# Kernel tuning notes

Hardware: AMD Instinct MI355X
Metric: run time of the kernel (lower is better)

Reference implementation:

```python
import jax, jax.numpy as jnp
import numpy as np

N_ATOMS = 100000
N_BONDS = 200000
N_MOLS = 4000
ATOMS_PER_MOL = 25
MAX_NB = 6
ATOM_FDIM = 133
BOND_FDIM = 14
HIDDEN = 300
DEPTH = 3


def setup_inputs() -> dict:
    key = jax.random.key(0)
    ks = jax.random.split(key, 8)
    f_atoms = jax.random.normal(ks[0], (N_ATOMS, ATOM_FDIM), dtype=jnp.float32)
    f_bonds = jax.random.normal(ks[1], (N_BONDS, BOND_FDIM), dtype=jnp.float32)
    # incoming-bond lists per atom (irregular gather targets)
    a2b = jax.random.randint(ks[2], (N_ATOMS, MAX_NB), 0, N_BONDS, dtype=jnp.int32)
    # source atom of each directed bond
    b2a = jax.random.randint(ks[3], (N_BONDS,), 0, N_ATOMS, dtype=jnp.int32)
    # reverse bond: directed bonds come in pairs (2i, 2i+1)
    b2revb = (jnp.arange(N_BONDS, dtype=jnp.int32) ^ 1)
    # contiguous [start, size] per molecule
    starts = jnp.arange(N_MOLS, dtype=jnp.int32) * ATOMS_PER_MOL
    sizes = jnp.full((N_MOLS,), ATOMS_PER_MOL, dtype=jnp.int32)
    a_scope = jnp.stack([starts, sizes], axis=1)
    W_i = jax.random.normal(ks[4], (HIDDEN, ATOM_FDIM + BOND_FDIM), dtype=jnp.float32) * 0.05
    W_h = jax.random.normal(ks[5], (HIDDEN, HIDDEN), dtype=jnp.float32) * 0.05
    W_o = jax.random.normal(ks[6], (HIDDEN, ATOM_FDIM + HIDDEN), dtype=jnp.float32) * 0.05
    b_o = jax.random.normal(ks[7], (HIDDEN,), dtype=jnp.float32) * 0.05
    return {"f_atoms": f_atoms, "f_bonds": f_bonds, "a2b": a2b, "b2a": b2a,
            "b2revb": b2revb, "a_scope": a_scope, "W_i": W_i, "W_h": W_h,
            "W_o": W_o, "b_o": b_o}


def reference(f_atoms, f_bonds, a2b, b2a, b2revb, a_scope, W_i, W_h, W_o, b_o):
    # initial directed-bond messages: [f_atoms[src], f_bonds] -> Linear -> ReLU
    input_feats = jnp.concatenate([f_atoms[b2a], f_bonds], axis=1)  # (E, 147)
    message = jax.nn.relu(input_feats @ W_i.T)  # (E, H)
    for _ in range(DEPTH - 1):
        nei_a_message = message[a2b].sum(axis=1)          # (V, H) gather+sum
        nei_message = nei_a_message[b2a] - message[b2revb]  # (E, H)
        message = jax.nn.relu(nei_message @ W_h.T)
    a_message = message[a2b].sum(axis=1)  # (V, H)
    atom_hiddens = jax.nn.relu(jnp.concatenate([f_atoms, a_message], axis=1) @ W_o.T + b_o)
    # vectorized scope mean-pool (scopes are contiguous ranges)
    starts = a_scope[:, 0]
    sizes = a_scope[:, 1]
    seg_ids = jnp.searchsorted(starts, jnp.arange(atom_hiddens.shape[0]), side='right') - 1
    sums = jax.ops.segment_sum(atom_hiddens, seg_ids, num_segments=N_MOLS)
    denom = jnp.maximum(sizes, 1).astype(atom_hiddens.dtype)[:, None]
    mol_vecs = jnp.where((sizes > 0)[:, None], sums / denom, 0.0)
    return mol_vecs
```

## Files before the change

### kernel.cpp

```cpp
#include <hip/hip_runtime.h>
#include <stdint.h>

#define N_ATOMS   100000
#define N_BONDS   200000
#define N_MOLS    4000
#define MAX_NB    6
#define ATOM_FDIM 133
#define BOND_FDIM 14
#define HIDDEN    300
#define NPAD      320

typedef __attribute__((ext_vector_type(8))) short          bf16x8;
typedef __attribute__((ext_vector_type(4))) float          f32x4;
typedef __attribute__((ext_vector_type(4))) unsigned int   u32x4;
typedef __attribute__((ext_vector_type(4), aligned(4))) float f32x4u;

static __device__ __forceinline__ float u2f(unsigned int u) {
  union { unsigned int u; float f; } v; v.u = u; return v.f;
}
static __device__ __forceinline__ unsigned int f2u(float f) {
  union { float f; unsigned int u; } v; v.f = f; return v.u;
}
static __device__ __forceinline__ float bflo(unsigned int u) { return u2f(u << 16); }
static __device__ __forceinline__ float bfhi(unsigned int u) { return u2f(u & 0xffff0000u); }
static __device__ __forceinline__ unsigned short f2bf_rn(float f) {
  unsigned int u = f2u(f);
  return (unsigned short)((u + 0x7fffu + ((u >> 16) & 1u)) >> 16);
}
static __device__ __forceinline__ unsigned int pack_rn(float lo, float hi) {
  return ((unsigned int)f2bf_rn(hi) << 16) | f2bf_rn(lo);
}

__global__ __launch_bounds__(256) void convw_kernel(
    const float* __restrict__ w, unsigned short* __restrict__ o,
    int Ksrc, int seg1, int src2off, int seg2dst, int seg2len, int KP) {
  int total = NPAD * KP;
  for (int idx = blockIdx.x * 256 + threadIdx.x; idx < total; idx += gridDim.x * 256) {
    int n = idx / KP, k = idx - n * KP;
    int src = -1;
    if (k < seg1) src = k;
    else if (k >= seg2dst && k < seg2dst + seg2len) src = src2off + (k - seg2dst);
    float v = (n < HIDDEN && src >= 0) ? w[(size_t)n * Ksrc + src] : 0.f;
    o[idx] = f2bf_rn(v);
  }
}

template<int KP, int MODE, bool RELU, bool BIAS>
__global__ __launch_bounds__(256, 3) void gemm_w(
    const float* __restrict__ F1, const float* __restrict__ F2,
    const unsigned short* __restrict__ S1, const int* __restrict__ gmap,
    const unsigned short* __restrict__ W, const float* __restrict__ bias,
    unsigned short* __restrict__ out, int M, int G) {
  constexpr int NST = KP / 32;
  constexpr int TG  = 5 * NST * 64;
  __shared__ __align__(16) unsigned short Wlds[TG * 8];

  const int nwg = gridDim.x, orig = blockIdx.x;
  const int xcd = orig & 7, q = nwg >> 3, r = nwg & 7;
  const int logical = (xcd < r ? xcd * (q + 1) : r * (q + 1) + (xcd - r) * q) + (orig >> 3);
  const int slice = logical & 3;
  const int mg    = logical >> 2;

  const int tid  = threadIdx.x;
  const int lane = tid & 63;
  const int wave = tid >> 6;
  const int ar   = lane & 15;
  const int kq   = lane >> 4;
  const int NS   = slice * 80;

  for (int g = tid; g < TG; g += 256) {
    int nf = g / (NST * 64);
    int rem = g - nf * NST * 64;
    int ks = rem >> 6, l = rem & 63;
    const unsigned short* src = W + (size_t)(NS + nf * 16 + (l & 15)) * KP + ks * 32 + (l >> 4) * 8;
    __builtin_amdgcn_global_load_lds(
        (const __attribute__((address_space(1))) void*)src,
        (__attribute__((address_space(3))) void*)((char*)Wlds + (size_t)g * 16), 16, 0, 0);
  }
  __syncthreads();

  const int nCh = (M + 63) >> 6;

  for (int c = wave; c < G; c += 4) {
    const int mc = mg * G + c;
    if (mc >= nCh) break;

    int rowm[4], gr[4];
#pragma unroll
    for (int m = 0; m < 4; m++) {
      int row = mc * 64 + m * 16 + ar;
      rowm[m] = (row < M) ? row : (M - 1);
      if (MODE == 1) gr[m] = gmap[rowm[m]];
    }

    f32x4 acc[4][5];
#pragma unroll
    for (int m = 0; m < 4; m++)
#pragma unroll
      for (int n = 0; n < 5; n++) acc[m][n] = (f32x4){0.f, 0.f, 0.f, 0.f};

    auto load_afrag = [&](int m, int ks) -> bf16x8 {
      union { u32x4 u; bf16x8 h; } cv;
      if (MODE == 0) {
        cv.u = *(const u32x4*)(S1 + (size_t)rowm[m] * KP + ks * 32 + kq * 8);
        return cv.h;
      }
      if (MODE == 2 && ks >= 5) {
        cv.u = *(const u32x4*)(S1 + (size_t)rowm[m] * NPAD + (ks - 5) * 32 + kq * 8);
        return cv.h;
      }
      const int k0 = ks * 32 + kq * 8;
      float v[8];
      if (MODE == 1 && ks == 5) {
#pragma unroll
        for (int j = 0; j < 8; j++) {
          int e = kq * 8 + j;
          v[j] = (e < BOND_FDIM) ? F2[(size_t)rowm[m] * BOND_FDIM + e] : 0.f;
        }
      } else {
        const int arow = (MODE == 1) ? gr[m] : rowm[m];
        if (k0 + 8 <= ATOM_FDIM) {
          const float* pa = F1 + (size_t)arow * ATOM_FDIM + k0;
          f32x4u v0 = *(const f32x4u*)pa;
          f32x4u v1 = *(const f32x4u*)(pa + 4);
#pragma unroll
          for (int j = 0; j < 4; j++) { v[j] = v0[j]; v[4 + j] = v1[j]; }
        } else {
#pragma unroll
          for (int j = 0; j < 8; j++) {
            int k = k0 + j;
            v[j] = (k < ATOM_FDIM) ? F1[(size_t)arow * ATOM_FDIM + k] : 0.f;
          }
        }
      }
      cv.u[0] = pack_rn(v[0], v[1]); cv.u[1] = pack_rn(v[2], v[3]);
      cv.u[2] = pack_rn(v[4], v[5]); cv.u[3] = pack_rn(v[6], v[7]);
      return cv.h;
    };

#pragma unroll
    for (int ks = 0; ks < NST; ks++) {
      bf16x8 af[4];
#pragma unroll
      for (int m = 0; m < 4; m++) af[m] = load_afrag(m, ks);
#pragma unroll
      for (int nf = 0; nf < 5; nf++) {
        bf16x8 bfr = *(const bf16x8*)&Wlds[((size_t)(nf * NST + ks) * 64 + lane) * 8];
#pragma unroll
        for (int m = 0; m < 4; m++)
          acc[m][nf] = __builtin_amdgcn_mfma_f32_16x16x32_bf16(af[m], bfr, acc[m][nf], 0, 0, 0);
      }
    }

#pragma unroll
    for (int m = 0; m < 4; m++) {
#pragma unroll
      for (int rr = 0; rr < 4; rr++) {
        int orow = mc * 64 + m * 16 + kq * 4 + rr;
        if (orow >= M) continue;
#pragma unroll
        for (int nf = 0; nf < 5; nf++) {
          int ocol = NS + nf * 16 + ar;
          float v = acc[m][nf][rr];
          if (BIAS) v += (ocol < HIDDEN) ? bias[ocol] : 0.f;
          if (RELU) v = v > 0.f ? v : 0.f;
          out[(size_t)orow * NPAD + ocol] = f2bf_rn(v);
        }
      }
    }
  }
}

__global__ __launch_bounds__(256) void agg_kernel(
    const unsigned short* __restrict__ src, const int* __restrict__ a2b,
    unsigned short* __restrict__ dst) {
  const int TPA = NPAD / 16;
  int idx = blockIdx.x * 256 + threadIdx.x;
  if (idx >= N_ATOMS * TPA) return;
  int a  = idx / TPA;
  int kc = (idx - a * TPA) * 16;
  int bidx[MAX_NB];
#pragma unroll
  for (int j = 0; j < MAX_NB; j++) bidx[j] = a2b[a * MAX_NB + j];
  float slo[8], shi[8];
#pragma unroll
  for (int t = 0; t < 8; t++) { slo[t] = 0.f; shi[t] = 0.f; }
#pragma unroll
  for (int j = 0; j < MAX_NB; j++) {
    const u32x4* p = (const u32x4*)(src + (size_t)bidx[j] * NPAD + kc);
    u32x4 v0 = p[0], v1 = p[1];
#pragma unroll
    for (int t = 0; t < 4; t++) {
      slo[t]     += bflo(v0[t]); shi[t]     += bfhi(v0[t]);
      slo[4 + t] += bflo(v1[t]); shi[4 + t] += bfhi(v1[t]);
    }
  }
  u32x4 o0, o1;
#pragma unroll
  for (int t = 0; t < 4; t++) { o0[t] = pack_rn(slo[t], shi[t]); o1[t] = pack_rn(slo[4 + t], shi[4 + t]); }
  u32x4* qp = (u32x4*)(dst + (size_t)a * NPAD + kc);
  qp[0] = o0; qp[1] = o1;
}

__global__ __launch_bounds__(256) void combineH_kernel(
    const unsigned short* __restrict__ neiZ, const unsigned short* Zh,
    const int* __restrict__ b2a, unsigned short* msg) {
  const int TPB = NPAD / 16;
  const int NPAIR = N_BONDS / 2;
  int idx = blockIdx.x * 256 + threadIdx.x;
  if (idx >= NPAIR * TPB) return;
  int p  = idx / TPB;
  int kc = (idx - p * TPB) * 16;
  int b0i = 2 * p, b1i = 2 * p + 1;
  int g0 = b2a[b0i], g1 = b2a[b1i];
  const u32x4* pn0 = (const u32x4*)(neiZ + (size_t)g0 * NPAD + kc);
  const u32x4* pn1 = (const u32x4*)(neiZ + (size_t)g1 * NPAD + kc);
  const u32x4* pz0 = (const u32x4*)(Zh + (size_t)b1i * NPAD + kc);
  const u32x4* pz1 = (const u32x4*)(Zh + (size_t)b0i * NPAD + kc);
  u32x4 n00 = pn0[0], n01 = pn0[1], n10 = pn1[0], n11 = pn1[1];
  u32x4 z00 = pz0[0], z01 = pz0[1], z10 = pz1[0], z11 = pz1[1];
  u32x4 o00, o01, o10, o11;
#pragma unroll
  for (int t = 0; t < 4; t++) {
    float a, c;
    a = bflo(n00[t]) - bflo(z00[t]); c = bfhi(n00[t]) - bfhi(z00[t]);
    o00[t] = pack_rn(a > 0.f ? a : 0.f, c > 0.f ? c : 0.f);
    a = bflo(n01[t]) - bflo(z01[t]); c = bfhi(n01[t]) - bfhi(z01[t]);
    o01[t] = pack_rn(a > 0.f ? a : 0.f, c > 0.f ? c : 0.f);
    a = bflo(n10[t]) - bflo(z10[t]); c = bfhi(n10[t]) - bfhi(z10[t]);
    o10[t] = pack_rn(a > 0.f ? a : 0.f, c > 0.f ? c : 0.f);
    a = bflo(n11[t]) - bflo(z11[t]); c = bfhi(n11[t]) - bfhi(z11[t]);
    o11[t] = pack_rn(a > 0.f ? a : 0.f, c > 0.f ? c : 0.f);
  }
  u32x4* q0 = (u32x4*)(msg + (size_t)b0i * NPAD + kc);
  u32x4* q1 = (u32x4*)(msg + (size_t)b1i * NPAD + kc);
  q0[0] = o00; q0[1] = o01; q1[0] = o10; q1[1] = o11;
}

__global__ __launch_bounds__(256) void readout_kernel(
    const unsigned short* __restrict__ hidden, const int* __restrict__ a_scope,
    float* __restrict__ out) {
  const int TPM = NPAD / 8;
  int idx = blockIdx.x * 256 + threadIdx.x;
  if (idx >= N_MOLS * TPM) return;
  int m = idx / TPM;
  int c = (idx - m * TPM) * 8;
  int start = a_scope[m * 2], size = a_scope[m * 2 + 1];
  float s[8];
#pragma unroll
  for (int t = 0; t < 8; t++) s[t] = 0.f;
  for (int i = 0; i < size; i++) {
    const u32x4 v = *(const u32x4*)(hidden + (size_t)(start + i) * NPAD + c);
#pragma unroll
    for (int t = 0; t < 4; t++) { s[2 * t] += bflo(v[t]); s[2 * t + 1] += bfhi(v[t]); }
  }
  float inv = (size > 0) ? 1.f / (float)size : 0.f;
#pragma unroll
  for (int t = 0; t < 8; t++) {
    int col = c + t;
    if (col < HIDDEN) out[(size_t)m * HIDDEN + col] = s[t] * inv;
  }
}

extern "C" void kernel_launch(void* const* d_in, const int* in_sizes, int n_in,
                              void* d_out, int out_size, void* d_ws, size_t ws_size,
                              hipStream_t stream) {
  const float* f_atoms = (const float*)d_in[0];
  const float* f_bonds = (const float*)d_in[1];
  const int*   a2b     = (const int*)d_in[2];
  const int*   b2a     = (const int*)d_in[3];
  const int*   a_scope = (const int*)d_in[5];
  const float* W_i     = (const float*)d_in[6];
  const float* W_h     = (const float*)d_in[7];
  const float* W_o     = (const float*)d_in[8];
  const float* b_o     = (const float*)d_in[9];
  float* out = (float*)d_out;

  char* ws = (char*)d_ws;
  size_t off = 0;
  auto alloc = [&](size_t bytes) { size_t o = off; off += (bytes + 255) & ~(size_t)255; return o; };
  unsigned short* P    = (unsigned short*)(ws + alloc((size_t)N_BONDS * NPAD * 2));
  unsigned short* Q    = (unsigned short*)(ws + alloc((size_t)N_BONDS * NPAD * 2));
  unsigned short* WiAB = (unsigned short*)(ws + alloc((size_t)NPAD * 192 * 2));
  unsigned short* Wh   = (unsigned short*)(ws + alloc((size_t)NPAD * 320 * 2));
  unsigned short* Wo   = (unsigned short*)(ws + alloc((size_t)NPAD * 480 * 2));

  convw_kernel<<<(NPAD * 192 + 255) / 256, 256, 0, stream>>>(W_i, WiAB, 147, 133, 133, 160, 14, 192);
  convw_kernel<<<(NPAD * 320 + 255) / 256, 256, 0, stream>>>(W_h, Wh, 300, 300, 0, 0, 0, 320);
  convw_kernel<<<(NPAD * 480 + 255) / 256, 256, 0, stream>>>(W_o, Wo, 433, 133, 133, 160, 300, 480);

  const int G = 8;
  const int nChB = (N_BONDS + 63) / 64;
  const int nChA = (N_ATOMS + 63) / 64;
  const int gridB = ((nChB + G - 1) / G) * 4;
  const int gridA = ((nChA + G - 1) / G) * 4;
  const int gagg = (N_ATOMS * (NPAD / 16) + 255) / 256;
  const int gpar = ((N_BONDS / 2) * (NPAD / 16) + 255) / 256;

  gemm_w<192, 1, true, false><<<gridB, 256, 0, stream>>>(
      f_atoms, f_bonds, nullptr, b2a, WiAB, nullptr, P, N_BONDS, G);

  gemm_w<320, 0, false, false><<<gridB, 256, 0, stream>>>(
      nullptr, nullptr, P, nullptr, Wh, nullptr, Q, N_BONDS, G);
  agg_kernel<<<gagg, 256, 0, stream>>>(Q, a2b, P);
  combineH_kernel<<<gpar, 256, 0, stream>>>(P, Q, b2a, Q);

  gemm_w<320, 0, false, false><<<gridB, 256, 0, stream>>>(
      nullptr, nullptr, Q, nullptr, Wh, nullptr, P, N_BONDS, G);
  agg_kernel<<<gagg, 256, 0, stream>>>(P, a2b, Q);
  combineH_kernel<<<gpar, 256, 0, stream>>>(Q, P, b2a, P);

  agg_kernel<<<gagg, 256, 0, stream>>>(P, a2b, Q);
  gemm_w<480, 2, true, true><<<gridA, 256, 0, stream>>>(
      f_atoms, nullptr, Q, nullptr, Wo, b_o, P, N_ATOMS, G);
  readout_kernel<<<(N_MOLS * (NPAD / 8) + 255) / 256, 256, 0, stream>>>(P, a_scope, out);
}
```

Baseline: 727.7 us.

## Stage activation tile in LDS and stream weights from global in GEMMs

Replaces the weight-stationary GEMM, where each workgroup held an 80-column weight slice in LDS and looped over eight 64-row chunks, with a one-tile-per-block design. Each 512-thread block now stages a 64-row activation tile (converted to bf16 where needed) in LDS, and eight waves split it into 2 row groups by 4 column slices, reading weight fragments directly from global/L2. This is meant to cut redundant activation reads across the four column slices and improve occupancy. The cost is that weights are re-read from cache by every block, and the large LDS tile (up to 61 KB for KP=480) limits how many blocks fit per CU.

```diff
diff --git a/kernel.cpp b/kernel.cpp
--- a/kernel.cpp
+++ b/kernel.cpp
@@ -11,9 +11,9 @@
 #define NPAD      320
 
 typedef __attribute__((ext_vector_type(8))) short          bf16x8;
+typedef __attribute__((ext_vector_type(8))) unsigned short u16x8;
 typedef __attribute__((ext_vector_type(4))) float          f32x4;
 typedef __attribute__((ext_vector_type(4))) unsigned int   u32x4;
-typedef __attribute__((ext_vector_type(4), aligned(4))) float f32x4u;
 
 static __device__ __forceinline__ float u2f(unsigned int u) {
   union { unsigned int u; float f; } v; v.u = u; return v.f;
@@ -46,126 +46,109 @@
 }
 
 template<int KP, int MODE, bool RELU, bool BIAS>
-__global__ __launch_bounds__(256, 3) void gemm_w(
+__global__ __launch_bounds__(512, 4) void gemm_hi(
     const float* __restrict__ F1, const float* __restrict__ F2,
     const unsigned short* __restrict__ S1, const int* __restrict__ gmap,
     const unsigned short* __restrict__ W, const float* __restrict__ bias,
-    unsigned short* __restrict__ out, int M, int G) {
+    unsigned short* __restrict__ out, int M) {
   constexpr int NST = KP / 32;
-  constexpr int TG  = 5 * NST * 64;
-  __shared__ __align__(16) unsigned short Wlds[TG * 8];
-
-  const int nwg = gridDim.x, orig = blockIdx.x;
-  const int xcd = orig & 7, q = nwg >> 3, r = nwg & 7;
-  const int logical = (xcd < r ? xcd * (q + 1) : r * (q + 1) + (xcd - r) * q) + (orig >> 3);
-  const int slice = logical & 3;
-  const int mg    = logical >> 2;
-
+  constexpr int TG  = KP * 8;
+  __shared__ __align__(16) unsigned short As[64 * KP];
+
+  const int b0   = blockIdx.x * 64;
   const int tid  = threadIdx.x;
   const int lane = tid & 63;
-  const int wave = tid >> 6;
-  const int ar   = lane & 15;
-  const int kq   = lane >> 4;
-  const int NS   = slice * 80;
-
-  for (int g = tid; g < TG; g += 256) {
-    int nf = g / (NST * 64);
-    int rem = g - nf * NST * 64;
-    int ks = rem >> 6, l = rem & 63;
-    const unsigned short* src = W + (size_t)(NS + nf * 16 + (l & 15)) * KP + ks * 32 + (l >> 4) * 8;
-    __builtin_amdgcn_global_load_lds(
-        (const __attribute__((address_space(1))) void*)src,
-        (__attribute__((address_space(3))) void*)((char*)Wlds + (size_t)g * 16), 16, 0, 0);
-  }
-  __syncthreads();
-
-  const int nCh = (M + 63) >> 6;
-
-  for (int c = wave; c < G; c += 4) {
-    const int mc = mg * G + c;
-    if (mc >= nCh) break;
-
-    int rowm[4], gr[4];
-#pragma unroll
-    for (int m = 0; m < 4; m++) {
-      int row = mc * 64 + m * 16 + ar;
-      rowm[m] = (row < M) ? row : (M - 1);
-      if (MODE == 1) gr[m] = gmap[rowm[m]];
-    }
-
-    f32x4 acc[4][5];
-#pragma unroll
-    for (int m = 0; m < 4; m++)
-#pragma unroll
-      for (int n = 0; n < 5; n++) acc[m][n] = (f32x4){0.f, 0.f, 0.f, 0.f};
-
-    auto load_afrag = [&](int m, int ks) -> bf16x8 {
-      union { u32x4 u; bf16x8 h; } cv;
-      if (MODE == 0) {
-        cv.u = *(const u32x4*)(S1 + (size_t)rowm[m] * KP + ks * 32 + kq * 8);
-        return cv.h;
+  const int wv   = tid >> 6;
+
+  if (MODE == 0) {
+#pragma unroll
+    for (int gb = wv * 64; gb < TG; gb += 512) {
+      const int cs = gb >> 6;
+      const int ae = cs * 8;
+      int row = b0 + lane; if (row >= M) row = M - 1;
+      const unsigned short* src = S1 + (size_t)row * KP + ae;
+      __builtin_amdgcn_global_load_lds(
+          (const __attribute__((address_space(1))) void*)src,
+          (__attribute__((address_space(3))) void*)((char*)As + (size_t)gb * 16), 16, 0, 0);
+    }
+  } else {
+    for (int g = tid; g < TG; g += 512) {
+      const int cs = g >> 6, r = g & 63, ae = cs * 8;
+      int row = b0 + r; if (row >= M) row = M - 1;
+      if (MODE == 2 && ae >= 160) {
+        const unsigned short* src = S1 + (size_t)row * NPAD + (ae - 160);
+        __builtin_amdgcn_global_load_lds(
+            (const __attribute__((address_space(1))) void*)src,
+            (__attribute__((address_space(3))) void*)((char*)As + (size_t)(g - lane) * 16), 16, 0, 0);
+        continue;
       }
-      if (MODE == 2 && ks >= 5) {
-        cv.u = *(const u32x4*)(S1 + (size_t)rowm[m] * NPAD + (ks - 5) * 32 + kq * 8);
-        return cv.h;
-      }
-      const int k0 = ks * 32 + kq * 8;
       float v[8];
-      if (MODE == 1 && ks == 5) {
+      if (MODE == 1) {
+        int grow = gmap[row];
 #pragma unroll
         for (int j = 0; j < 8; j++) {
-          int e = kq * 8 + j;
-          v[j] = (e < BOND_FDIM) ? F2[(size_t)rowm[m] * BOND_FDIM + e] : 0.f;
+          int k = ae + j;
+          float x = 0.f;
+          if (k < ATOM_FDIM) x = F1[(size_t)grow * ATOM_FDIM + k];
+          else if (k >= 160 && k < 160 + BOND_FDIM) x = F2[(size_t)row * BOND_FDIM + (k - 160)];
+          v[j] = x;
         }
       } else {
-        const int arow = (MODE == 1) ? gr[m] : rowm[m];
-        if (k0 + 8 <= ATOM_FDIM) {
-          const float* pa = F1 + (size_t)arow * ATOM_FDIM + k0;
-          f32x4u v0 = *(const f32x4u*)pa;
-          f32x4u v1 = *(const f32x4u*)(pa + 4);
-#pragma unroll
-          for (int j = 0; j < 4; j++) { v[j] = v0[j]; v[4 + j] = v1[j]; }
-        } else {
-#pragma unroll
-          for (int j = 0; j < 8; j++) {
-            int k = k0 + j;
-            v[j] = (k < ATOM_FDIM) ? F1[(size_t)arow * ATOM_FDIM + k] : 0.f;
-          }
+#pragma unroll
+        for (int j = 0; j < 8; j++) {
+          int k = ae + j;
+          v[j] = (k < ATOM_FDIM) ? F1[(size_t)row * ATOM_FDIM + k] : 0.f;
         }
       }
-      cv.u[0] = pack_rn(v[0], v[1]); cv.u[1] = pack_rn(v[2], v[3]);
-      cv.u[2] = pack_rn(v[4], v[5]); cv.u[3] = pack_rn(v[6], v[7]);
-      return cv.h;
-    };
-
-#pragma unroll
-    for (int ks = 0; ks < NST; ks++) {
-      bf16x8 af[4];
-#pragma unroll
-      for (int m = 0; m < 4; m++) af[m] = load_afrag(m, ks);
+      u32x4 o;
+      o[0] = pack_rn(v[0], v[1]); o[1] = pack_rn(v[2], v[3]);
+      o[2] = pack_rn(v[4], v[5]); o[3] = pack_rn(v[6], v[7]);
+      *(u32x4*)((char*)As + (size_t)g * 16) = o;
+    }
+  }
+  __syncthreads();
+
+  const int rg = wv >> 2;
+  const int NS = (wv & 3) * 80;
+  const int ar = lane & 15, kq = lane >> 4;
+
+  f32x4 acc[2][5];
+#pragma unroll
+  for (int m = 0; m < 2; m++)
+#pragma unroll
+    for (int n = 0; n < 5; n++) acc[m][n] = (f32x4){0.f, 0.f, 0.f, 0.f};
+
+  const unsigned short* Wl = W + (size_t)(NS + ar) * KP + kq * 8;
+
+#pragma unroll
+  for (int ks = 0; ks < NST; ks++) {
+    bf16x8 af[2];
+#pragma unroll
+    for (int m = 0; m < 2; m++)
+      af[m] = *(const bf16x8*)((const char*)As
+               + (size_t)((ks * 4 + kq) * 64 + rg * 32 + m * 16 + ar) * 16);
+#pragma unroll
+    for (int nf = 0; nf < 5; nf++) {
+      bf16x8 bfr = *(const bf16x8*)(Wl + (size_t)nf * 16 * KP + ks * 32);
+#pragma unroll
+      for (int m = 0; m < 2; m++)
+        acc[m][nf] = __builtin_amdgcn_mfma_f32_16x16x32_bf16(af[m], bfr, acc[m][nf], 0, 0, 0);
+    }
+  }
+
+#pragma unroll
+  for (int m = 0; m < 2; m++) {
+#pragma unroll
+    for (int rr = 0; rr < 4; rr++) {
+      int orow = b0 + rg * 32 + m * 16 + kq * 4 + rr;
+      if (orow >= M) continue;
 #pragma unroll
       for (int nf = 0; nf < 5; nf++) {
-        bf16x8 bfr = *(const bf16x8*)&Wlds[((size_t)(nf * NST + ks) * 64 + lane) * 8];
-#pragma unroll
-        for (int m = 0; m < 4; m++)
-          acc[m][nf] = __builtin_amdgcn_mfma_f32_16x16x32_bf16(af[m], bfr, acc[m][nf], 0, 0, 0);
-      }
-    }
-
-#pragma unroll
-    for (int m = 0; m < 4; m++) {
-#pragma unroll
-      for (int rr = 0; rr < 4; rr++) {
-        int orow = mc * 64 + m * 16 + kq * 4 + rr;
-        if (orow >= M) continue;
-#pragma unroll
-        for (int nf = 0; nf < 5; nf++) {
-          int ocol = NS + nf * 16 + ar;
-          float v = acc[m][nf][rr];
-          if (BIAS) v += (ocol < HIDDEN) ? bias[ocol] : 0.f;
-          if (RELU) v = v > 0.f ? v : 0.f;
-          out[(size_t)orow * NPAD + ocol] = f2bf_rn(v);
-        }
+        int ocol = NS + nf * 16 + ar;
+        float v = acc[m][nf][rr];
+        if (BIAS) v += (ocol < HIDDEN) ? bias[ocol] : 0.f;
+        if (RELU) v = v > 0.f ? v : 0.f;
+        out[(size_t)orow * NPAD + ocol] = f2bf_rn(v);
       }
     }
   }
@@ -289,29 +272,26 @@
   convw_kernel<<<(NPAD * 320 + 255) / 256, 256, 0, stream>>>(W_h, Wh, 300, 300, 0, 0, 0, 320);
   convw_kernel<<<(NPAD * 480 + 255) / 256, 256, 0, stream>>>(W_o, Wo, 433, 133, 133, 160, 300, 480);
 
-  const int G = 8;
-  const int nChB = (N_BONDS + 63) / 64;
-  const int nChA = (N_ATOMS + 63) / 64;
-  const int gridB = ((nChB + G - 1) / G) * 4;
-  const int gridA = ((nChA + G - 1) / G) * 4;
+  const int gridB = (N_BONDS + 63) / 64;
+  const int gridA = (N_ATOMS + 63) / 64;
   const int gagg = (N_ATOMS * (NPAD / 16) + 255) / 256;
   const int gpar = ((N_BONDS / 2) * (NPAD / 16) + 255) / 256;
 
-  gemm_w<192, 1, true, false><<<gridB, 256, 0, stream>>>(
-      f_atoms, f_bonds, nullptr, b2a, WiAB, nullptr, P, N_BONDS, G);
-
-  gemm_w<320, 0, false, false><<<gridB, 256, 0, stream>>>(
-      nullptr, nullptr, P, nullptr, Wh, nullptr, Q, N_BONDS, G);
+  gemm_hi<192, 1, true, false><<<gridB, 512, 0, stream>>>(
+      f_atoms, f_bonds, nullptr, b2a, WiAB, nullptr, P, N_BONDS);
+
+  gemm_hi<320, 0, false, false><<<gridB, 512, 0, stream>>>(
+      nullptr, nullptr, P, nullptr, Wh, nullptr, Q, N_BONDS);
   agg_kernel<<<gagg, 256, 0, stream>>>(Q, a2b, P);
   combineH_kernel<<<gpar, 256, 0, stream>>>(P, Q, b2a, Q);
 
-  gemm_w<320, 0, false, false><<<gridB, 256, 0, stream>>>(
-      nullptr, nullptr, Q, nullptr, Wh, nullptr, P, N_BONDS, G);
+  gemm_hi<320, 0, false, false><<<gridB, 512, 0, stream>>>(
+      nullptr, nullptr, Q, nullptr, Wh, nullptr, P, N_BONDS);
   agg_kernel<<<gagg, 256, 0, stream>>>(P, a2b, Q);
   combineH_kernel<<<gpar, 256, 0, stream>>>(Q, P, b2a, P);
 
   agg_kernel<<<gagg, 256, 0, stream>>>(P, a2b, Q);
-  gemm_w<480, 2, true, true><<<gridA, 256, 0, stream>>>(
-      f_atoms, nullptr, Q, nullptr, Wo, b_o, P, N_ATOMS, G);
+  gemm_hi<480, 2, true, true><<<gridA, 512, 0, stream>>>(
+      f_atoms, nullptr, Q, nullptr, Wo, b_o, P, N_ATOMS);
   readout_kernel<<<(N_MOLS * (NPAD / 8) + 255) / 256, 256, 0, stream>>>(P, a_scope, out);
 }
```

Result: slower. 951.3 us (+30.7%).
